# Kernel tuning notes

Measured on AMD Instinct MI355X. Metric: run time of the kernel, lower is better.

Reference implementation:

```python
import jax, jax.numpy as jnp
import numpy as np

SIGMA = 1.0
TOP_K = 4

def setup_inputs() -> dict:
    key = jax.random.key(0)
    k1, k2, k3, k4 = jax.random.split(key, 4)
    B, N, IN_DIM, OUT_DIM, P = 2, 4096, 128, 128, 3
    x = jax.random.normal(k1, (B, N, IN_DIM), dtype=jnp.float32)
    pos = jax.random.normal(k2, (B, N, P), dtype=jnp.float32)
    # Linear(in_dim, out_dim): W [in_dim, out_dim], b [out_dim]
    lim = 1.0 / np.sqrt(IN_DIM)
    W = jax.random.uniform(k3, (IN_DIM, OUT_DIM), minval=-lim, maxval=lim, dtype=jnp.float32)
    b = jax.random.uniform(k4, (OUT_DIM,), minval=-lim, maxval=lim, dtype=jnp.float32)
    return {"x": x, "pos": pos, "W": W, "b": b}

def reference(x, pos, W, b):
    B, N, _ = x.shape
    # pairwise distances [B, N, N]
    pos_diff = pos[:, :, None, :] - pos[:, None, :, :]
    dist = jnp.sqrt(jnp.sum(pos_diff ** 2, axis=-1) + 1e-8)
    adj = jnp.exp(-dist ** 2 / (2.0 * SIGMA ** 2))
    # top-k mask along last dim
    _, indices = jax.lax.top_k(adj, TOP_K)  # [B, N, k]
    b_idx = jnp.arange(B)[:, None, None]
    n_idx = jnp.arange(N)[None, :, None]
    mask = jnp.zeros_like(adj).at[b_idx, n_idx, indices].set(1.0)
    adj = adj * mask
    adj = adj / (jnp.sum(adj, axis=-1, keepdims=True) + 1e-8)
    # weighted aggregation + linear
    out = jnp.einsum('bnm,bmd->bnd', adj, x)
    return out @ W + b
```

## Files before the change

kernel.cpp:

```cpp
#include <hip/hip_runtime.h>
#include <hip/hip_bf16.h>

#define NPTS 4096
#define NROWS 8192
#define DIM 128
#define GEMM_BLOCKS 1024

typedef __attribute__((ext_vector_type(8))) short bf16x8;
typedef __attribute__((ext_vector_type(4))) float f32x4;

__global__ __launch_bounds__(256) void k1_prep_gemm(const float* __restrict__ x,
                                                    const float* __restrict__ pos,
                                                    const float* __restrict__ W,
                                                    float4* __restrict__ pos4,
                                                    __hip_bfloat16* __restrict__ xWb) {
    int b = blockIdx.x;
    if (b >= GEMM_BLOCKS) {
        int t = (b - GEMM_BLOCKS) * 256 + threadIdx.x;
        const float* p = pos + (size_t)t * 3;
        pos4[t] = make_float4(p[0], p[1], p[2], 0.f);
        return;
    }
    int wave = threadIdx.x >> 6;
    int lane = threadIdx.x & 63;
    int tile = b * 4 + wave;
    int m0 = (tile >> 3) << 4;
    int n0 = (tile & 7) << 4;
    int r = lane & 15;
    int kg = lane >> 4;
    const float* xr = x + (size_t)(m0 + r) * DIM + kg * 8;
    const float* wc = W + (size_t)(kg * 8) * DIM + (n0 + r);
    f32x4 acc = {0.f, 0.f, 0.f, 0.f};
    union { __hip_bfloat16 h; short s; } u;
#pragma unroll
    for (int kb = 0; kb < 4; ++kb) {
        float4 a0 = *(const float4*)(xr + kb * 32);
        float4 a1 = *(const float4*)(xr + kb * 32 + 4);
        bf16x8 af, bf;
        u.h = __float2bfloat16(a0.x); af[0] = u.s;
        u.h = __float2bfloat16(a0.y); af[1] = u.s;
        u.h = __float2bfloat16(a0.z); af[2] = u.s;
        u.h = __float2bfloat16(a0.w); af[3] = u.s;
        u.h = __float2bfloat16(a1.x); af[4] = u.s;
        u.h = __float2bfloat16(a1.y); af[5] = u.s;
        u.h = __float2bfloat16(a1.z); af[6] = u.s;
        u.h = __float2bfloat16(a1.w); af[7] = u.s;
#pragma unroll
        for (int i = 0; i < 8; ++i) {
            u.h = __float2bfloat16(wc[(size_t)(kb * 32 + i) * DIM]);
            bf[i] = u.s;
        }
        acc = __builtin_amdgcn_mfma_f32_16x16x32_bf16(af, bf, acc, 0, 0, 0);
    }
    int col = n0 + r;
    int rbase = m0 + (kg << 2);
#pragma unroll
    for (int reg = 0; reg < 4; ++reg)
        xWb[(size_t)(rbase + reg) * DIM + col] = __float2bfloat16(acc[reg]);
}

__device__ __forceinline__ double mkkey(float d2, int j) {
    return __longlong_as_double(__double_as_longlong((double)d2) |
                                (unsigned long long)(unsigned)j);
}

__device__ __forceinline__ void kins(double& k0, double& k1, double& k2,
                                     double& k3, double s) {
    double c = fmax(k0, s); k0 = fmin(k0, s);
    double t = fmax(k1, c); k1 = fmin(k1, c); c = t;
    t = fmax(k2, c);        k2 = fmin(k2, c); c = t;
    k3 = fmin(k3, c);
}

__device__ __forceinline__ void kmerge(double& a0, double& a1, double& a2,
                                       double& a3, double b0, double b1,
                                       double b2, double b3) {
    double m0 = fmin(a0, b3), m1 = fmin(a1, b2);
    double m2 = fmin(a2, b1), m3 = fmin(a3, b0);
    double t0 = fmin(m0, m2), t2 = fmax(m0, m2);
    double t1 = fmin(m1, m3), t3 = fmax(m1, m3);
    a0 = fmin(t0, t1); a1 = fmax(t0, t1);
    a2 = fmin(t2, t3); a3 = fmax(t2, t3);
}

__global__ __launch_bounds__(256) void topk_agg(const float4* __restrict__ pos4,
                                                const __hip_bfloat16* __restrict__ xWb,
                                                const float* __restrict__ bias,
                                                float* __restrict__ out) {
    int lane = threadIdx.x & 63;
    int wave = threadIdx.x >> 6;
    int rowbase = blockIdx.x * 2;
    int batch = rowbase >> 12;
    int ibase = rowbase & (NPTS - 1);
    const float4* pb = pos4 + (size_t)batch * NPTS;

    float4 q0 = pb[ibase], q1 = pb[ibase + 1];
    const double INF = __builtin_inf();
    double a0 = INF, a1 = INF, a2 = INF, a3 = INF;
    double b0 = INF, b1 = INF, b2 = INF, b3 = INF;

    int jbase = (wave << 10) + lane;
#pragma unroll 4
    for (int t = 0; t < 16; ++t) {
        int j = jbase + (t << 6);
        float4 p = pb[j];
        float dx = q0.x - p.x, dy = q0.y - p.y, dz = q0.z - p.z;
        float d2 = fmaf(dx, dx, fmaf(dy, dy, dz * dz));
        kins(a0, a1, a2, a3, mkkey(d2, j));
        dx = q1.x - p.x; dy = q1.y - p.y; dz = q1.z - p.z;
        d2 = fmaf(dx, dx, fmaf(dy, dy, dz * dz));
        kins(b0, b1, b2, b3, mkkey(d2, j));
    }

#pragma unroll
    for (int off = 1; off < 64; off <<= 1) {
        double p0 = __shfl_xor(a0, off), p1 = __shfl_xor(a1, off);
        double p2 = __shfl_xor(a2, off), p3 = __shfl_xor(a3, off);
        kmerge(a0, a1, a2, a3, p0, p1, p2, p3);
        p0 = __shfl_xor(b0, off); p1 = __shfl_xor(b1, off);
        p2 = __shfl_xor(b2, off); p3 = __shfl_xor(b3, off);
        kmerge(b0, b1, b2, b3, p0, p1, p2, p3);
    }

    __shared__ double lds[4][2][4];
    if (lane == 0) {
        lds[wave][0][0] = a0; lds[wave][0][1] = a1;
        lds[wave][0][2] = a2; lds[wave][0][3] = a3;
        lds[wave][1][0] = b0; lds[wave][1][1] = b1;
        lds[wave][1][2] = b2; lds[wave][1][3] = b3;
    }
    __syncthreads();
    if (wave) return;

#pragma unroll
    for (int qq = 1; qq < 4; ++qq) {
        kmerge(a0, a1, a2, a3, lds[qq][0][0], lds[qq][0][1],
                               lds[qq][0][2], lds[qq][0][3]);
        kmerge(b0, b1, b2, b3, lds[qq][1][0], lds[qq][1][1],
                               lds[qq][1][2], lds[qq][1][3]);
    }

    int c = lane << 1;
    float2 bb = *(const float2*)(bias + c);
    const unsigned short* xu = (const unsigned short*)xWb;
    size_t bbase = ((size_t)batch * NPTS) << 7;
#pragma unroll
    for (int k = 0; k < 2; ++k) {
        double k0 = k ? b0 : a0, k1 = k ? b1 : a1;
        double k2 = k ? b2 : a2, k3 = k ? b3 : a3;
        unsigned i0 = (unsigned)__double_as_longlong(k0) & 0xFFFu;
        unsigned i1 = (unsigned)__double_as_longlong(k1) & 0xFFFu;
        unsigned i2 = (unsigned)__double_as_longlong(k2) & 0xFFFu;
        unsigned i3 = (unsigned)__double_as_longlong(k3) & 0xFFFu;
        float d0 = (float)k0, d1 = (float)k1, d2 = (float)k2, d3 = (float)k3;
        float w0 = __expf(-(d0 + 1e-8f) * 0.5f);
        float w1 = __expf(-(d1 + 1e-8f) * 0.5f);
        float w2 = __expf(-(d2 + 1e-8f) * 0.5f);
        float w3 = __expf(-(d3 + 1e-8f) * 0.5f);
        float inv = 1.0f / (w0 + w1 + w2 + w3 + 1e-8f);
        w0 *= inv; w1 *= inv; w2 *= inv; w3 *= inv;
        ushort2 g0 = *(const ushort2*)(xu + bbase + ((size_t)i0 << 7) + c);
        ushort2 g1 = *(const ushort2*)(xu + bbase + ((size_t)i1 << 7) + c);
        ushort2 g2 = *(const ushort2*)(xu + bbase + ((size_t)i2 << 7) + c);
        ushort2 g3 = *(const ushort2*)(xu + bbase + ((size_t)i3 << 7) + c);
        float ox = bb.x + w0 * __uint_as_float((unsigned)g0.x << 16)
                        + w1 * __uint_as_float((unsigned)g1.x << 16)
                        + w2 * __uint_as_float((unsigned)g2.x << 16)
                        + w3 * __uint_as_float((unsigned)g3.x << 16);
        float oy = bb.y + w0 * __uint_as_float((unsigned)g0.y << 16)
                        + w1 * __uint_as_float((unsigned)g1.y << 16)
                        + w2 * __uint_as_float((unsigned)g2.y << 16)
                        + w3 * __uint_as_float((unsigned)g3.y << 16);
        *(float2*)(out + (((size_t)(rowbase + k)) << 7) + c) = make_float2(ox, oy);
    }
}

extern "C" void kernel_launch(void* const* d_in, const int* in_sizes, int n_in,
                              void* d_out, int out_size, void* d_ws, size_t ws_size,
                              hipStream_t stream) {
    const float* x    = (const float*)d_in[0];
    const float* pos  = (const float*)d_in[1];
    const float* W    = (const float*)d_in[2];
    const float* bias = (const float*)d_in[3];
    float* out = (float*)d_out;

    char* ws = (char*)d_ws;
    __hip_bfloat16* xWb = (__hip_bfloat16*)ws;
    float4* pos4 = (float4*)(ws + (size_t)NROWS * DIM * 2);

    k1_prep_gemm<<<GEMM_BLOCKS + NROWS / 256, 256, 0, stream>>>(x, pos, W, pos4, xWb);
    topk_agg<<<NROWS / 2, 256, 0, stream>>>(pos4, xWb, bias, out);
}
```

Baseline: 91.13 us.

## Replace brute-force top-k with uniform grid spatial binning and neighbor-cell search

Positions are binned into a 32^3 uniform grid per batch using atomics, and each point searches its 27 neighboring cells, expanding to a 5x5x5 shell or falling back to a wave-wide brute force when the result cannot be certified. Overflow points beyond per-cell capacity go to a list that is scanned exhaustively. This replaces the O(N^2) distance scan with near-linear work. In exchange it adds a memset, atomics and an extra kernel launch, and per-thread work is divergent.

```diff
diff --git a/kernel.cpp b/kernel.cpp
--- a/kernel.cpp
+++ b/kernel.cpp
@@ -5,29 +5,44 @@
 #define NROWS 8192
 #define DIM 128
 #define GEMM_BLOCKS 1024
+#define HCELL 0.25f
+#define LOW (-4.0f)
+#define CAP 16
+#define NCELLS 32768
+#define OVCAP 4096
 
 typedef __attribute__((ext_vector_type(8))) short bf16x8;
 typedef __attribute__((ext_vector_type(4))) float f32x4;
 
-__global__ __launch_bounds__(256) void k1_prep_gemm(const float* __restrict__ x,
-                                                    const float* __restrict__ pos,
-                                                    const float* __restrict__ W,
-                                                    float4* __restrict__ pos4,
-                                                    __hip_bfloat16* __restrict__ xWb) {
+__device__ __forceinline__ int cellcoord(float v) {
+    int c = (int)floorf((v - LOW) / HCELL);
+    return c < 0 ? 0 : (c > 31 ? 31 : c);
+}
+
+__global__ __launch_bounds__(256) void k1_gemm_bin(const float* __restrict__ x,
+        const float* __restrict__ pos, const float* __restrict__ W,
+        __hip_bfloat16* __restrict__ xWb, unsigned* __restrict__ cellCnt,
+        float4* __restrict__ cellPts, unsigned* __restrict__ ovfCnt,
+        float4* __restrict__ ovfList) {
     int b = blockIdx.x;
     if (b >= GEMM_BLOCKS) {
         int t = (b - GEMM_BLOCKS) * 256 + threadIdx.x;
+        int batch = t >> 12;
         const float* p = pos + (size_t)t * 3;
-        pos4[t] = make_float4(p[0], p[1], p[2], 0.f);
+        float px = p[0], py = p[1], pz = p[2];
+        int cx = cellcoord(px), cy = cellcoord(py), cz = cellcoord(pz);
+        int cid = ((batch * 32 + cz) * 32 + cy) * 32 + cx;
+        unsigned slot = atomicAdd(&cellCnt[cid], 1u);
+        float4 rec = make_float4(px, py, pz, __uint_as_float((unsigned)(t & (NPTS - 1))));
+        if (slot < CAP) cellPts[(size_t)cid * CAP + slot] = rec;
+        else { unsigned o = atomicAdd(&ovfCnt[batch], 1u);
+               if (o < OVCAP) ovfList[(size_t)batch * OVCAP + o] = rec; }
         return;
     }
-    int wave = threadIdx.x >> 6;
-    int lane = threadIdx.x & 63;
+    int wave = threadIdx.x >> 6, lane = threadIdx.x & 63;
     int tile = b * 4 + wave;
-    int m0 = (tile >> 3) << 4;
-    int n0 = (tile & 7) << 4;
-    int r = lane & 15;
-    int kg = lane >> 4;
+    int m0 = (tile >> 3) << 4, n0 = (tile & 7) << 4;
+    int r = lane & 15, kg = lane >> 4;
     const float* xr = x + (size_t)(m0 + r) * DIM + kg * 8;
     const float* wc = W + (size_t)(kg * 8) * DIM + (n0 + r);
     f32x4 acc = {0.f, 0.f, 0.f, 0.f};
@@ -52,8 +67,7 @@
         }
         acc = __builtin_amdgcn_mfma_f32_16x16x32_bf16(af, bf, acc, 0, 0, 0);
     }
-    int col = n0 + r;
-    int rbase = m0 + (kg << 2);
+    int col = n0 + r, rbase = m0 + (kg << 2);
 #pragma unroll
     for (int reg = 0; reg < 4; ++reg)
         xWb[(size_t)(rbase + reg) * DIM + col] = __float2bfloat16(acc[reg]);
@@ -63,7 +77,6 @@
     return __longlong_as_double(__double_as_longlong((double)d2) |
                                 (unsigned long long)(unsigned)j);
 }
-
 __device__ __forceinline__ void kins(double& k0, double& k1, double& k2,
                                      double& k3, double s) {
     double c = fmax(k0, s); k0 = fmin(k0, s);
@@ -71,7 +84,6 @@
     t = fmax(k2, c);        k2 = fmin(k2, c); c = t;
     k3 = fmin(k3, c);
 }
-
 __device__ __forceinline__ void kmerge(double& a0, double& a1, double& a2,
                                        double& a3, double b0, double b1,
                                        double b2, double b3) {
@@ -83,71 +95,143 @@
     a2 = fmin(t2, t3); a3 = fmax(t2, t3);
 }
 
-__global__ __launch_bounds__(256) void topk_agg(const float4* __restrict__ pos4,
-                                                const __hip_bfloat16* __restrict__ xWb,
-                                                const float* __restrict__ bias,
-                                                float* __restrict__ out) {
+__global__ __launch_bounds__(256) void knn(const unsigned* __restrict__ cellCnt,
+        const float4* __restrict__ cellPts, const unsigned* __restrict__ ovfCnt,
+        const float4* __restrict__ ovfList, const float* __restrict__ pos,
+        float4* __restrict__ res) {
+    int g = blockIdx.x * 256 + threadIdx.x;
     int lane = threadIdx.x & 63;
-    int wave = threadIdx.x >> 6;
-    int rowbase = blockIdx.x * 2;
-    int batch = rowbase >> 12;
-    int ibase = rowbase & (NPTS - 1);
-    const float4* pb = pos4 + (size_t)batch * NPTS;
-
-    float4 q0 = pb[ibase], q1 = pb[ibase + 1];
+    bool active = false, resolved = false, bruted = false;
+    float4 me = make_float4(0.f, 0.f, 0.f, 0.f);
+    int batch;
+    if (g < (1 << 20)) {
+        int cid = g >> 4, slot = g & 15;
+        unsigned cnt = cellCnt[cid];
+        unsigned cc = cnt < CAP ? cnt : CAP;
+        batch = cid >> 15;
+        active = (unsigned)slot < cc;
+        if (active) me = cellPts[(size_t)cid * CAP + slot];
+    } else {
+        int o = g - (1 << 20);
+        batch = o >> 12;
+        int oslot = o & 4095;
+        unsigned oc = ovfCnt[batch]; oc = oc < OVCAP ? oc : OVCAP;
+        active = (unsigned)oslot < oc;
+        if (active) me = ovfList[(size_t)batch * OVCAP + oslot];
+    }
+    float qx = me.x, qy = me.y, qz = me.z;
     const double INF = __builtin_inf();
-    double a0 = INF, a1 = INF, a2 = INF, a3 = INF;
-    double b0 = INF, b1 = INF, b2 = INF, b3 = INF;
-
-    int jbase = (wave << 10) + lane;
+    double k0 = INF, k1 = INF, k2 = INF, k3 = INF;
+    int cx = cellcoord(qx), cy = cellcoord(qy), cz = cellcoord(qz);
+    const unsigned* cb = cellCnt + (size_t)batch * NCELLS;
+    const float4* pb4 = cellPts + (size_t)batch * NCELLS * CAP;
+
+    if (active) {
+        unsigned cnts[27]; int lids[27];
+#pragma unroll
+        for (int i = 0; i < 27; ++i) {
+            int dz = i / 9 - 1, dy = (i / 3) % 3 - 1, dx = i % 3 - 1;
+            int nx = cx + dx, ny = cy + dy, nz = cz + dz;
+            bool ok = (unsigned)nx < 32u && (unsigned)ny < 32u && (unsigned)nz < 32u;
+            int lid = (nz * 32 + ny) * 32 + nx;
+            lids[i] = lid;
+            cnts[i] = ok ? cb[lid] : 0u;
+        }
 #pragma unroll 4
-    for (int t = 0; t < 16; ++t) {
-        int j = jbase + (t << 6);
-        float4 p = pb[j];
-        float dx = q0.x - p.x, dy = q0.y - p.y, dz = q0.z - p.z;
-        float d2 = fmaf(dx, dx, fmaf(dy, dy, dz * dz));
-        kins(a0, a1, a2, a3, mkkey(d2, j));
-        dx = q1.x - p.x; dy = q1.y - p.y; dz = q1.z - p.z;
-        d2 = fmaf(dx, dx, fmaf(dy, dy, dz * dz));
-        kins(b0, b1, b2, b3, mkkey(d2, j));
-    }
-
-#pragma unroll
-    for (int off = 1; off < 64; off <<= 1) {
-        double p0 = __shfl_xor(a0, off), p1 = __shfl_xor(a1, off);
-        double p2 = __shfl_xor(a2, off), p3 = __shfl_xor(a3, off);
-        kmerge(a0, a1, a2, a3, p0, p1, p2, p3);
-        p0 = __shfl_xor(b0, off); p1 = __shfl_xor(b1, off);
-        p2 = __shfl_xor(b2, off); p3 = __shfl_xor(b3, off);
-        kmerge(b0, b1, b2, b3, p0, p1, p2, p3);
-    }
-
-    __shared__ double lds[4][2][4];
-    if (lane == 0) {
-        lds[wave][0][0] = a0; lds[wave][0][1] = a1;
-        lds[wave][0][2] = a2; lds[wave][0][3] = a3;
-        lds[wave][1][0] = b0; lds[wave][1][1] = b1;
-        lds[wave][1][2] = b2; lds[wave][1][3] = b3;
-    }
-    __syncthreads();
-    if (wave) return;
-
-#pragma unroll
-    for (int qq = 1; qq < 4; ++qq) {
-        kmerge(a0, a1, a2, a3, lds[qq][0][0], lds[qq][0][1],
-                               lds[qq][0][2], lds[qq][0][3]);
-        kmerge(b0, b1, b2, b3, lds[qq][1][0], lds[qq][1][1],
-                               lds[qq][1][2], lds[qq][1][3]);
-    }
-
-    int c = lane << 1;
-    float2 bb = *(const float2*)(bias + c);
-    const unsigned short* xu = (const unsigned short*)xWb;
-    size_t bbase = ((size_t)batch * NPTS) << 7;
-#pragma unroll
-    for (int k = 0; k < 2; ++k) {
-        double k0 = k ? b0 : a0, k1 = k ? b1 : a1;
-        double k2 = k ? b2 : a2, k3 = k ? b3 : a3;
+        for (int i = 0; i < 27; ++i) {
+            unsigned c = cnts[i] < CAP ? cnts[i] : CAP;
+            const float4* cp = pb4 + (size_t)lids[i] * CAP;
+            for (unsigned s = 0; s < c; ++s) {
+                float4 p = cp[s];
+                float ddx = qx - p.x, ddy = qy - p.y, ddz = qz - p.z;
+                float d2 = fmaf(ddx, ddx, fmaf(ddy, ddy, ddz * ddz));
+                kins(k0, k1, k2, k3, mkkey(d2, (int)__float_as_uint(p.w)));
+            }
+        }
+        {
+            float dbox = 1e30f;
+            if (cx - 1 > 0)  dbox = fminf(dbox, qx - (LOW + (cx - 1) * HCELL));
+            if (cx + 1 < 31) dbox = fminf(dbox, (LOW + (cx + 2) * HCELL) - qx);
+            if (cy - 1 > 0)  dbox = fminf(dbox, qy - (LOW + (cy - 1) * HCELL));
+            if (cy + 1 < 31) dbox = fminf(dbox, (LOW + (cy + 2) * HCELL) - qy);
+            if (cz - 1 > 0)  dbox = fminf(dbox, qz - (LOW + (cz - 1) * HCELL));
+            if (cz + 1 < 31) dbox = fminf(dbox, (LOW + (cz + 2) * HCELL) - qz);
+            resolved = ((float)k3 < 0.999f * dbox * dbox);
+        }
+        if (!resolved) {
+            for (int sz = -2; sz <= 2; ++sz) {
+                int nz = cz + sz;
+                bool zok = (unsigned)nz < 32u;
+                unsigned c2[25]; int l2[25];
+#pragma unroll
+                for (int i = 0; i < 25; ++i) {
+                    int dy = i / 5 - 2, dx = i % 5 - 2;
+                    bool inner = sz >= -1 && sz <= 1 && dy >= -1 && dy <= 1 &&
+                                 dx >= -1 && dx <= 1;
+                    int ny = cy + dy, nx = cx + dx;
+                    bool ok = zok && !inner && (unsigned)ny < 32u && (unsigned)nx < 32u;
+                    int lid = (nz * 32 + ny) * 32 + nx;
+                    l2[i] = lid;
+                    c2[i] = ok ? cb[lid] : 0u;
+                }
+#pragma unroll 4
+                for (int i = 0; i < 25; ++i) {
+                    unsigned c = c2[i] < CAP ? c2[i] : CAP;
+                    const float4* cp = pb4 + (size_t)l2[i] * CAP;
+                    for (unsigned s = 0; s < c; ++s) {
+                        float4 p = cp[s];
+                        float ddx = qx - p.x, ddy = qy - p.y, ddz = qz - p.z;
+                        float d2 = fmaf(ddx, ddx, fmaf(ddy, ddy, ddz * ddz));
+                        kins(k0, k1, k2, k3, mkkey(d2, (int)__float_as_uint(p.w)));
+                    }
+                }
+            }
+            float dbox = 1e30f;
+            if (cx - 2 > 0)  dbox = fminf(dbox, qx - (LOW + (cx - 2) * HCELL));
+            if (cx + 2 < 31) dbox = fminf(dbox, (LOW + (cx + 3) * HCELL) - qx);
+            if (cy - 2 > 0)  dbox = fminf(dbox, qy - (LOW + (cy - 2) * HCELL));
+            if (cy + 2 < 31) dbox = fminf(dbox, (LOW + (cy + 3) * HCELL) - qy);
+            if (cz - 2 > 0)  dbox = fminf(dbox, qz - (LOW + (cz - 2) * HCELL));
+            if (cz + 2 < 31) dbox = fminf(dbox, (LOW + (cz + 3) * HCELL) - qz);
+            resolved = ((float)k3 < 0.999f * dbox * dbox);
+        }
+    }
+
+    unsigned long long mask = __ballot(active && !resolved);
+    while (mask) {
+        int src = __ffsll((unsigned long long)mask) - 1;
+        mask &= mask - 1;
+        float bx = __shfl(qx, src), by = __shfl(qy, src), bz = __shfl(qz, src);
+        double c0 = INF, c1 = INF, c2 = INF, c3 = INF;
+        const float* pp = pos + (size_t)batch * NPTS * 3;
+        for (int t = 0; t < 64; ++t) {
+            int j = t * 64 + lane;
+            float px = pp[3 * j], py = pp[3 * j + 1], pz = pp[3 * j + 2];
+            float ddx = bx - px, ddy = by - py, ddz = bz - pz;
+            float d2 = fmaf(ddx, ddx, fmaf(ddy, ddy, ddz * ddz));
+            kins(c0, c1, c2, c3, mkkey(d2, j));
+        }
+#pragma unroll
+        for (int off = 1; off < 64; off <<= 1) {
+            double p0 = __shfl_xor(c0, off), p1 = __shfl_xor(c1, off);
+            double p2 = __shfl_xor(c2, off), p3 = __shfl_xor(c3, off);
+            kmerge(c0, c1, c2, c3, p0, p1, p2, p3);
+        }
+        if (lane == src) { k0 = c0; k1 = c1; k2 = c2; k3 = c3; bruted = true; }
+    }
+
+    if (active && !bruted) {
+        unsigned oc = ovfCnt[batch]; oc = oc < OVCAP ? oc : OVCAP;
+        const float4* ol = ovfList + (size_t)batch * OVCAP;
+        for (unsigned o = 0; o < oc; ++o) {
+            float4 p = ol[o];
+            float ddx = qx - p.x, ddy = qy - p.y, ddz = qz - p.z;
+            float d2 = fmaf(ddx, ddx, fmaf(ddy, ddy, ddz * ddz));
+            kins(k0, k1, k2, k3, mkkey(d2, (int)__float_as_uint(p.w)));
+        }
+    }
+
+    if (active) {
         unsigned i0 = (unsigned)__double_as_longlong(k0) & 0xFFFu;
         unsigned i1 = (unsigned)__double_as_longlong(k1) & 0xFFFu;
         unsigned i2 = (unsigned)__double_as_longlong(k2) & 0xFFFu;
@@ -158,20 +242,42 @@
         float w2 = __expf(-(d2 + 1e-8f) * 0.5f);
         float w3 = __expf(-(d3 + 1e-8f) * 0.5f);
         float inv = 1.0f / (w0 + w1 + w2 + w3 + 1e-8f);
-        w0 *= inv; w1 *= inv; w2 *= inv; w3 *= inv;
+        int row = batch * NPTS + (int)__float_as_uint(me.w);
+        res[2 * row] = make_float4(__uint_as_float(i0), __uint_as_float(i1),
+                                   __uint_as_float(i2), __uint_as_float(i3));
+        res[2 * row + 1] = make_float4(w0 * inv, w1 * inv, w2 * inv, w3 * inv);
+    }
+}
+
+__global__ __launch_bounds__(256) void agg_out(const float4* __restrict__ res,
+        const __hip_bfloat16* __restrict__ xWb, const float* __restrict__ bias,
+        float* __restrict__ out) {
+    int lane = threadIdx.x & 63, wave = threadIdx.x >> 6;
+    int rowbase = blockIdx.x * 8 + wave * 2;
+    int batch = rowbase >> 12;
+    int c = lane << 1;
+    float2 bb = *(const float2*)(bias + c);
+    const unsigned short* xu = (const unsigned short*)xWb;
+    size_t bbase = ((size_t)batch * NPTS) << 7;
+#pragma unroll
+    for (int k = 0; k < 2; ++k) {
+        int row = rowbase + k;
+        float4 ri = res[2 * row], rw = res[2 * row + 1];
+        unsigned i0 = __float_as_uint(ri.x), i1 = __float_as_uint(ri.y);
+        unsigned i2 = __float_as_uint(ri.z), i3 = __float_as_uint(ri.w);
         ushort2 g0 = *(const ushort2*)(xu + bbase + ((size_t)i0 << 7) + c);
         ushort2 g1 = *(const ushort2*)(xu + bbase + ((size_t)i1 << 7) + c);
         ushort2 g2 = *(const ushort2*)(xu + bbase + ((size_t)i2 << 7) + c);
         ushort2 g3 = *(const ushort2*)(xu + bbase + ((size_t)i3 << 7) + c);
-        float ox = bb.x + w0 * __uint_as_float((unsigned)g0.x << 16)
-                        + w1 * __uint_as_float((unsigned)g1.x << 16)
-                        + w2 * __uint_as_float((unsigned)g2.x << 16)
-                        + w3 * __uint_as_float((unsigned)g3.x << 16);
-        float oy = bb.y + w0 * __uint_as_float((unsigned)g0.y << 16)
-                        + w1 * __uint_as_float((unsigned)g1.y << 16)
-                        + w2 * __uint_as_float((unsigned)g2.y << 16)
-                        + w3 * __uint_as_float((unsigned)g3.y << 16);
-        *(float2*)(out + (((size_t)(rowbase + k)) << 7) + c) = make_float2(ox, oy);
+        float ox = bb.x + rw.x * __uint_as_float((unsigned)g0.x << 16)
+                        + rw.y * __uint_as_float((unsigned)g1.x << 16)
+                        + rw.z * __uint_as_float((unsigned)g2.x << 16)
+                        + rw.w * __uint_as_float((unsigned)g3.x << 16);
+        float oy = bb.y + rw.x * __uint_as_float((unsigned)g0.y << 16)
+                        + rw.y * __uint_as_float((unsigned)g1.y << 16)
+                        + rw.z * __uint_as_float((unsigned)g2.y << 16)
+                        + rw.w * __uint_as_float((unsigned)g3.y << 16);
+        *(float2*)(out + ((size_t)row << 7) + c) = make_float2(ox, oy);
     }
 }
 
@@ -186,8 +292,16 @@
 
     char* ws = (char*)d_ws;
     __hip_bfloat16* xWb = (__hip_bfloat16*)ws;
-    float4* pos4 = (float4*)(ws + (size_t)NROWS * DIM * 2);
-
-    k1_prep_gemm<<<GEMM_BLOCKS + NROWS / 256, 256, 0, stream>>>(x, pos, W, pos4, xWb);
-    topk_agg<<<NROWS / 2, 256, 0, stream>>>(pos4, xWb, bias, out);
-}
+    float4* res        = (float4*)(ws + 2097152);
+    unsigned* cellCnt  = (unsigned*)(ws + 2359296);
+    unsigned* ovfCnt   = (unsigned*)(ws + 2621440);
+    float4* cellPts    = (float4*)(ws + 2621456);
+    float4* ovfList    = (float4*)(ws + 2621456 + 16777216);
+
+    hipMemsetAsync(ws + 2359296, 0, 262160, stream);
+    k1_gemm_bin<<<GEMM_BLOCKS + NROWS / 256, 256, 0, stream>>>(
+        x, pos, W, xWb, cellCnt, cellPts, ovfCnt, ovfList);
+    knn<<<(1 << 20) / 256 + 2 * OVCAP / 256, 256, 0, stream>>>(
+        cellCnt, cellPts, ovfCnt, ovfList, pos, res);
+    agg_out<<<NROWS / 8, 256, 0, stream>>>(res, xWb, bias, out);
+}
```

Result: slower. 136.2 us (+49.5%).

## Replace brute-force kNN with uniform grid binning and local cell search

Applied to the files above, without the earlier changes.

Points are binned into a 32^3 uniform grid per batch with atomic slot allocation, plus an overflow list for full cells. Each query wave then scans only the 5x5x5 neighbouring cells and checks that its 4th-nearest distance lies within the searched box. If not, it falls back to a full brute-force scan. This avoids the O(N^2) distance sweep, at the cost of a memset, atomics, irregular per-lane loop lengths and scattered gathers.

```diff
diff --git a/kernel.cpp b/kernel.cpp
--- a/kernel.cpp
+++ b/kernel.cpp
@@ -5,29 +5,44 @@
 #define NROWS 8192
 #define DIM 128
 #define GEMM_BLOCKS 1024
+#define HCELL 0.25f
+#define LOW (-4.0f)
+#define CAP 16
+#define NCELLS 32768
+#define OVCAP 4096
 
 typedef __attribute__((ext_vector_type(8))) short bf16x8;
 typedef __attribute__((ext_vector_type(4))) float f32x4;
 
-__global__ __launch_bounds__(256) void k1_prep_gemm(const float* __restrict__ x,
-                                                    const float* __restrict__ pos,
-                                                    const float* __restrict__ W,
-                                                    float4* __restrict__ pos4,
-                                                    __hip_bfloat16* __restrict__ xWb) {
+__device__ __forceinline__ int cellcoord(float v) {
+    int c = (int)floorf((v - LOW) / HCELL);
+    return c < 0 ? 0 : (c > 31 ? 31 : c);
+}
+
+__global__ __launch_bounds__(256) void k1_gemm_bin(const float* __restrict__ x,
+        const float* __restrict__ pos, const float* __restrict__ W,
+        __hip_bfloat16* __restrict__ xWb, unsigned* __restrict__ cellCnt,
+        float4* __restrict__ cellPts, unsigned* __restrict__ ovfCnt,
+        float4* __restrict__ ovfList) {
     int b = blockIdx.x;
     if (b >= GEMM_BLOCKS) {
         int t = (b - GEMM_BLOCKS) * 256 + threadIdx.x;
+        int batch = t >> 12;
         const float* p = pos + (size_t)t * 3;
-        pos4[t] = make_float4(p[0], p[1], p[2], 0.f);
+        float px = p[0], py = p[1], pz = p[2];
+        int cx = cellcoord(px), cy = cellcoord(py), cz = cellcoord(pz);
+        int cid = ((batch * 32 + cz) * 32 + cy) * 32 + cx;
+        unsigned slot = atomicAdd(&cellCnt[cid], 1u);
+        float4 rec = make_float4(px, py, pz, __uint_as_float((unsigned)(t & (NPTS - 1))));
+        if (slot < CAP) cellPts[(size_t)cid * CAP + slot] = rec;
+        else { unsigned o = atomicAdd(&ovfCnt[batch], 1u);
+               if (o < OVCAP) ovfList[(size_t)batch * OVCAP + o] = rec; }
         return;
     }
-    int wave = threadIdx.x >> 6;
-    int lane = threadIdx.x & 63;
+    int wave = threadIdx.x >> 6, lane = threadIdx.x & 63;
     int tile = b * 4 + wave;
-    int m0 = (tile >> 3) << 4;
-    int n0 = (tile & 7) << 4;
-    int r = lane & 15;
-    int kg = lane >> 4;
+    int m0 = (tile >> 3) << 4, n0 = (tile & 7) << 4;
+    int r = lane & 15, kg = lane >> 4;
     const float* xr = x + (size_t)(m0 + r) * DIM + kg * 8;
     const float* wc = W + (size_t)(kg * 8) * DIM + (n0 + r);
     f32x4 acc = {0.f, 0.f, 0.f, 0.f};
@@ -52,8 +67,7 @@
         }
         acc = __builtin_amdgcn_mfma_f32_16x16x32_bf16(af, bf, acc, 0, 0, 0);
     }
-    int col = n0 + r;
-    int rbase = m0 + (kg << 2);
+    int col = n0 + r, rbase = m0 + (kg << 2);
 #pragma unroll
     for (int reg = 0; reg < 4; ++reg)
         xWb[(size_t)(rbase + reg) * DIM + col] = __float2bfloat16(acc[reg]);
@@ -63,7 +77,6 @@
     return __longlong_as_double(__double_as_longlong((double)d2) |
                                 (unsigned long long)(unsigned)j);
 }
-
 __device__ __forceinline__ void kins(double& k0, double& k1, double& k2,
                                      double& k3, double s) {
     double c = fmax(k0, s); k0 = fmin(k0, s);
@@ -71,7 +84,6 @@
     t = fmax(k2, c);        k2 = fmin(k2, c); c = t;
     k3 = fmin(k3, c);
 }
-
 __device__ __forceinline__ void kmerge(double& a0, double& a1, double& a2,
                                        double& a3, double b0, double b1,
                                        double b2, double b3) {
@@ -83,96 +95,115 @@
     a2 = fmin(t2, t3); a3 = fmax(t2, t3);
 }
 
-__global__ __launch_bounds__(256) void topk_agg(const float4* __restrict__ pos4,
-                                                const __hip_bfloat16* __restrict__ xWb,
-                                                const float* __restrict__ bias,
-                                                float* __restrict__ out) {
+__global__ __launch_bounds__(256) void knn_agg(const unsigned* __restrict__ cellCnt,
+        const float4* __restrict__ cellPts, const unsigned* __restrict__ ovfCnt,
+        const float4* __restrict__ ovfList, const float* __restrict__ pos,
+        const __hip_bfloat16* __restrict__ xWb, const float* __restrict__ bias,
+        float* __restrict__ out) {
     int lane = threadIdx.x & 63;
     int wave = threadIdx.x >> 6;
-    int rowbase = blockIdx.x * 2;
-    int batch = rowbase >> 12;
-    int ibase = rowbase & (NPTS - 1);
-    const float4* pb = pos4 + (size_t)batch * NPTS;
-
-    float4 q0 = pb[ibase], q1 = pb[ibase + 1];
+    int row = blockIdx.x * 4 + wave;
+    int batch = row >> 12;
+    int qi = row & (NPTS - 1);
+    const float* pb = pos + (size_t)batch * NPTS * 3;
+    float qx = pb[3 * qi], qy = pb[3 * qi + 1], qz = pb[3 * qi + 2];
+    int cx = cellcoord(qx), cy = cellcoord(qy), cz = cellcoord(qz);
+    const unsigned* cb = cellCnt + (size_t)batch * NCELLS;
+    const float4* pb4 = cellPts + (size_t)batch * NCELLS * CAP;
+
     const double INF = __builtin_inf();
-    double a0 = INF, a1 = INF, a2 = INF, a3 = INF;
-    double b0 = INF, b1 = INF, b2 = INF, b3 = INF;
-
-    int jbase = (wave << 10) + lane;
+    double k0 = INF, k1 = INF, k2 = INF, k3 = INF;
+
+#pragma unroll
+    for (int mm = 0; mm < 2; ++mm) {
+        int m = lane + mm * 64;
+        if (m < 125) {
+            int dz = m / 25 - 2, dy = (m / 5) % 5 - 2, dx = m % 5 - 2;
+            int nx = cx + dx, ny = cy + dy, nz = cz + dz;
+            if ((unsigned)nx < 32u && (unsigned)ny < 32u && (unsigned)nz < 32u) {
+                int lid = (nz * 32 + ny) * 32 + nx;
+                unsigned c = cb[lid]; c = c < CAP ? c : CAP;
+                const float4* cp = pb4 + (size_t)lid * CAP;
+                for (unsigned s = 0; s < c; ++s) {
+                    float4 p = cp[s];
+                    float ddx = qx - p.x, ddy = qy - p.y, ddz = qz - p.z;
+                    float d2 = fmaf(ddx, ddx, fmaf(ddy, ddy, ddz * ddz));
+                    kins(k0, k1, k2, k3, mkkey(d2, (int)__float_as_uint(p.w)));
+                }
+            }
+        }
+    }
+#pragma unroll
+    for (int off = 1; off < 64; off <<= 1) {
+        double p0 = __shfl_xor(k0, off), p1 = __shfl_xor(k1, off);
+        double p2 = __shfl_xor(k2, off), p3 = __shfl_xor(k3, off);
+        kmerge(k0, k1, k2, k3, p0, p1, p2, p3);
+    }
+
+    float dbox = 1e30f;
+    if (cx - 2 > 0)  dbox = fminf(dbox, qx - (LOW + (cx - 2) * HCELL));
+    if (cx + 2 < 31) dbox = fminf(dbox, (LOW + (cx + 3) * HCELL) - qx);
+    if (cy - 2 > 0)  dbox = fminf(dbox, qy - (LOW + (cy - 2) * HCELL));
+    if (cy + 2 < 31) dbox = fminf(dbox, (LOW + (cy + 3) * HCELL) - qy);
+    if (cz - 2 > 0)  dbox = fminf(dbox, qz - (LOW + (cz - 2) * HCELL));
+    if (cz + 2 < 31) dbox = fminf(dbox, (LOW + (cz + 3) * HCELL) - qz);
+    bool resolved = ((float)k3 < 0.999f * dbox * dbox) && ((float)k3 < 1e29f);
+
+    if (!resolved) {
+        k0 = INF; k1 = INF; k2 = INF; k3 = INF;
 #pragma unroll 4
-    for (int t = 0; t < 16; ++t) {
-        int j = jbase + (t << 6);
-        float4 p = pb[j];
-        float dx = q0.x - p.x, dy = q0.y - p.y, dz = q0.z - p.z;
-        float d2 = fmaf(dx, dx, fmaf(dy, dy, dz * dz));
-        kins(a0, a1, a2, a3, mkkey(d2, j));
-        dx = q1.x - p.x; dy = q1.y - p.y; dz = q1.z - p.z;
-        d2 = fmaf(dx, dx, fmaf(dy, dy, dz * dz));
-        kins(b0, b1, b2, b3, mkkey(d2, j));
-    }
-
-#pragma unroll
-    for (int off = 1; off < 64; off <<= 1) {
-        double p0 = __shfl_xor(a0, off), p1 = __shfl_xor(a1, off);
-        double p2 = __shfl_xor(a2, off), p3 = __shfl_xor(a3, off);
-        kmerge(a0, a1, a2, a3, p0, p1, p2, p3);
-        p0 = __shfl_xor(b0, off); p1 = __shfl_xor(b1, off);
-        p2 = __shfl_xor(b2, off); p3 = __shfl_xor(b3, off);
-        kmerge(b0, b1, b2, b3, p0, p1, p2, p3);
-    }
-
-    __shared__ double lds[4][2][4];
-    if (lane == 0) {
-        lds[wave][0][0] = a0; lds[wave][0][1] = a1;
-        lds[wave][0][2] = a2; lds[wave][0][3] = a3;
-        lds[wave][1][0] = b0; lds[wave][1][1] = b1;
-        lds[wave][1][2] = b2; lds[wave][1][3] = b3;
-    }
-    __syncthreads();
-    if (wave) return;
-
-#pragma unroll
-    for (int qq = 1; qq < 4; ++qq) {
-        kmerge(a0, a1, a2, a3, lds[qq][0][0], lds[qq][0][1],
-                               lds[qq][0][2], lds[qq][0][3]);
-        kmerge(b0, b1, b2, b3, lds[qq][1][0], lds[qq][1][1],
-                               lds[qq][1][2], lds[qq][1][3]);
-    }
-
+        for (int t = 0; t < NPTS / 64; ++t) {
+            int j = t * 64 + lane;
+            float px = pb[3 * j], py = pb[3 * j + 1], pz = pb[3 * j + 2];
+            float ddx = qx - px, ddy = qy - py, ddz = qz - pz;
+            float d2 = fmaf(ddx, ddx, fmaf(ddy, ddy, ddz * ddz));
+            kins(k0, k1, k2, k3, mkkey(d2, j));
+        }
+#pragma unroll
+        for (int off = 1; off < 64; off <<= 1) {
+            double p0 = __shfl_xor(k0, off), p1 = __shfl_xor(k1, off);
+            double p2 = __shfl_xor(k2, off), p3 = __shfl_xor(k3, off);
+            kmerge(k0, k1, k2, k3, p0, p1, p2, p3);
+        }
+    } else {
+        unsigned oc = ovfCnt[batch]; oc = oc < OVCAP ? oc : OVCAP;
+        const float4* ol = ovfList + (size_t)batch * OVCAP;
+        for (unsigned o = 0; o < oc; ++o) {
+            float4 p = ol[o];
+            float ddx = qx - p.x, ddy = qy - p.y, ddz = qz - p.z;
+            float d2 = fmaf(ddx, ddx, fmaf(ddy, ddy, ddz * ddz));
+            kins(k0, k1, k2, k3, mkkey(d2, (int)__float_as_uint(p.w)));
+        }
+    }
+
+    unsigned i0 = (unsigned)__double_as_longlong(k0) & 0xFFFu;
+    unsigned i1 = (unsigned)__double_as_longlong(k1) & 0xFFFu;
+    unsigned i2 = (unsigned)__double_as_longlong(k2) & 0xFFFu;
+    unsigned i3 = (unsigned)__double_as_longlong(k3) & 0xFFFu;
+    float d0 = (float)k0, d1 = (float)k1, d2 = (float)k2, d3 = (float)k3;
+    float w0 = __expf(-(d0 + 1e-8f) * 0.5f);
+    float w1 = __expf(-(d1 + 1e-8f) * 0.5f);
+    float w2 = __expf(-(d2 + 1e-8f) * 0.5f);
+    float w3 = __expf(-(d3 + 1e-8f) * 0.5f);
+    float inv = 1.0f / (w0 + w1 + w2 + w3 + 1e-8f);
+    w0 *= inv; w1 *= inv; w2 *= inv; w3 *= inv;
     int c = lane << 1;
     float2 bb = *(const float2*)(bias + c);
     const unsigned short* xu = (const unsigned short*)xWb;
     size_t bbase = ((size_t)batch * NPTS) << 7;
-#pragma unroll
-    for (int k = 0; k < 2; ++k) {
-        double k0 = k ? b0 : a0, k1 = k ? b1 : a1;
-        double k2 = k ? b2 : a2, k3 = k ? b3 : a3;
-        unsigned i0 = (unsigned)__double_as_longlong(k0) & 0xFFFu;
-        unsigned i1 = (unsigned)__double_as_longlong(k1) & 0xFFFu;
-        unsigned i2 = (unsigned)__double_as_longlong(k2) & 0xFFFu;
-        unsigned i3 = (unsigned)__double_as_longlong(k3) & 0xFFFu;
-        float d0 = (float)k0, d1 = (float)k1, d2 = (float)k2, d3 = (float)k3;
-        float w0 = __expf(-(d0 + 1e-8f) * 0.5f);
-        float w1 = __expf(-(d1 + 1e-8f) * 0.5f);
-        float w2 = __expf(-(d2 + 1e-8f) * 0.5f);
-        float w3 = __expf(-(d3 + 1e-8f) * 0.5f);
-        float inv = 1.0f / (w0 + w1 + w2 + w3 + 1e-8f);
-        w0 *= inv; w1 *= inv; w2 *= inv; w3 *= inv;
-        ushort2 g0 = *(const ushort2*)(xu + bbase + ((size_t)i0 << 7) + c);
-        ushort2 g1 = *(const ushort2*)(xu + bbase + ((size_t)i1 << 7) + c);
-        ushort2 g2 = *(const ushort2*)(xu + bbase + ((size_t)i2 << 7) + c);
-        ushort2 g3 = *(const ushort2*)(xu + bbase + ((size_t)i3 << 7) + c);
-        float ox = bb.x + w0 * __uint_as_float((unsigned)g0.x << 16)
-                        + w1 * __uint_as_float((unsigned)g1.x << 16)
-                        + w2 * __uint_as_float((unsigned)g2.x << 16)
-                        + w3 * __uint_as_float((unsigned)g3.x << 16);
-        float oy = bb.y + w0 * __uint_as_float((unsigned)g0.y << 16)
-                        + w1 * __uint_as_float((unsigned)g1.y << 16)
-                        + w2 * __uint_as_float((unsigned)g2.y << 16)
-                        + w3 * __uint_as_float((unsigned)g3.y << 16);
-        *(float2*)(out + (((size_t)(rowbase + k)) << 7) + c) = make_float2(ox, oy);
-    }
+    ushort2 g0 = *(const ushort2*)(xu + bbase + ((size_t)i0 << 7) + c);
+    ushort2 g1 = *(const ushort2*)(xu + bbase + ((size_t)i1 << 7) + c);
+    ushort2 g2 = *(const ushort2*)(xu + bbase + ((size_t)i2 << 7) + c);
+    ushort2 g3 = *(const ushort2*)(xu + bbase + ((size_t)i3 << 7) + c);
+    float ox = bb.x + w0 * __uint_as_float((unsigned)g0.x << 16)
+                    + w1 * __uint_as_float((unsigned)g1.x << 16)
+                    + w2 * __uint_as_float((unsigned)g2.x << 16)
+                    + w3 * __uint_as_float((unsigned)g3.x << 16);
+    float oy = bb.y + w0 * __uint_as_float((unsigned)g0.y << 16)
+                    + w1 * __uint_as_float((unsigned)g1.y << 16)
+                    + w2 * __uint_as_float((unsigned)g2.y << 16)
+                    + w3 * __uint_as_float((unsigned)g3.y << 16);
+    *(float2*)(out + ((size_t)row << 7) + c) = make_float2(ox, oy);
 }
 
 extern "C" void kernel_launch(void* const* d_in, const int* in_sizes, int n_in,
@@ -186,8 +217,14 @@
 
     char* ws = (char*)d_ws;
     __hip_bfloat16* xWb = (__hip_bfloat16*)ws;
-    float4* pos4 = (float4*)(ws + (size_t)NROWS * DIM * 2);
-
-    k1_prep_gemm<<<GEMM_BLOCKS + NROWS / 256, 256, 0, stream>>>(x, pos, W, pos4, xWb);
-    topk_agg<<<NROWS / 2, 256, 0, stream>>>(pos4, xWb, bias, out);
-}
+    unsigned* cellCnt  = (unsigned*)(ws + 2097152);
+    unsigned* ovfCnt   = (unsigned*)(ws + 2359296);
+    float4* cellPts    = (float4*)(ws + 2359312);
+    float4* ovfList    = (float4*)(ws + 2359312 + 16777216);
+
+    hipMemsetAsync(ws + 2097152, 0, 262160, stream);
+    k1_gemm_bin<<<GEMM_BLOCKS + NROWS / 256, 256, 0, stream>>>(
+        x, pos, W, xWb, cellCnt, cellPts, ovfCnt, ovfList);
+    knn_agg<<<NROWS / 4, 256, 0, stream>>>(
+        cellCnt, cellPts, ovfCnt, ovfList, pos, xWb, bias, out);
+}
```

Measured after the change: 84.97 us, median of 2. 6.8% less time.
